# Kernel optimization log

Hardware: AMD Instinct MI355X
Metric: run time of the kernel (lower is better)

The kernel has to match this reference:

```python
import jax, jax.numpy as jnp
import numpy as np

NUM_TOKENS = 4096
LATENT_DIM = 128
BETA = 0.25
TEMP = 1.0  # temperature buffer (eval mode, no annealing)


def _l2_normalize(x, eps=1e-12):
    n = jnp.linalg.norm(x, axis=-1, keepdims=True)
    return x / jnp.maximum(n, eps)


def setup_inputs() -> dict:
    key = jax.random.key(0)
    k1, k2 = jax.random.split(key)
    latent = jax.random.normal(k1, (16, 1024, LATENT_DIM), dtype=jnp.float32)
    # codebook init: uniform(-1/num_tokens, 1/num_tokens) as in the module
    codebook_w = jax.random.uniform(
        k2, (NUM_TOKENS, LATENT_DIM), dtype=jnp.float32,
        minval=-1.0 / NUM_TOKENS, maxval=1.0 / NUM_TOKENS)
    return {"latent": latent, "codebook_w": codebook_w}


def reference(latent, codebook_w):
    B, S, D = latent.shape
    K = codebook_w.shape[0]
    flat = latent.reshape(-1, D)                      # [N, D]
    N = flat.shape[0]

    # cosine similarity between normalized inputs and codes
    cos = _l2_normalize(flat) @ _l2_normalize(codebook_w).T  # [N, K]

    # squared euclidean distances
    dist = (jnp.sum(flat * flat, axis=1, keepdims=True)
            - 2.0 * (flat @ codebook_w.T)
            + jnp.sum(codebook_w * codebook_w, axis=1))       # [N, K]

    soft = jax.nn.softmax(-dist / max(TEMP, 1e-5), axis=-1)   # [N, K]
    idx = jnp.argmax(soft, axis=-1)                            # [N]
    hard = jax.nn.one_hot(idx, K, dtype=flat.dtype)            # [N, K]
    # straight-through assignment
    assign = hard + soft - jax.lax.stop_gradient(soft)

    sel_cos = jnp.take_along_axis(cos, idx[:, None], axis=1).mean()

    # codebook self pairwise euclidean distances (K x K)
    sq = jnp.sum(codebook_w * codebook_w, axis=1)
    d2 = sq[:, None] + sq[None, :] - 2.0 * (codebook_w @ codebook_w.T)
    d = jnp.sqrt(jnp.maximum(d2, 0.0))
    # diagonal is exactly 0 after clamp, so off-diagonal mean = sum/(K*(K-1))
    avg_euclidean = d.sum() / (K * (K - 1))
    min_euclidean = jnp.min(jnp.where(jnp.eye(K, dtype=bool), jnp.inf, d))

    quantized = (assign @ codebook_w).reshape(B, S, D)
    commitment_loss = BETA * jnp.mean((jax.lax.stop_gradient(latent) - quantized) ** 2)
    codebook_loss = jnp.mean((latent - jax.lax.stop_gradient(quantized)) ** 2)
    quantized_st = latent + jax.lax.stop_gradient(quantized - latent)

    avg_probs = hard.mean(axis=0)
    perplexity = jnp.exp(-jnp.sum(avg_probs * jnp.log(avg_probs + 1e-10)))

    return (quantized_st, idx, commitment_loss, codebook_loss,
            perplexity, sel_cos, avg_euclidean, min_euclidean)
```

## Files before the change

kernel.cpp:

```cpp
#include <hip/hip_runtime.h>
#include <hip/hip_fp16.h>
#include <math.h>

#define NTOK 16384
#define KCB  4096
#define DIM  128
#define NG8  (KCB / 8)

typedef short bf16x8 __attribute__((ext_vector_type(8)));
typedef float f32x4  __attribute__((ext_vector_type(4)));

static __device__ inline unsigned short rne_bf16(float f) {
  unsigned u = __float_as_uint(f);
  return (unsigned short)((u + 0x7FFFu + ((u >> 16) & 1u)) >> 16);
}


__global__ __launch_bounds__(256) void k_convert(const float* __restrict__ cb,
                                                 unsigned short* __restrict__ cbh) {
  const int base = (blockIdx.x * 256 + threadIdx.x) * 8;
  float4 v0 = *(const float4*)(cb + base);
  float4 v1 = *(const float4*)(cb + base + 4);
  ushort4 o0, o1;
  o0.x = rne_bf16(v0.x); o0.y = rne_bf16(v0.y); o0.z = rne_bf16(v0.z); o0.w = rne_bf16(v0.w);
  o1.x = rne_bf16(v1.x); o1.y = rne_bf16(v1.y); o1.z = rne_bf16(v1.z); o1.w = rne_bf16(v1.w);
  *(ushort4*)(cbh + base) = o0;
  *(ushort4*)(cbh + base + 4) = o1;
}

__global__ __launch_bounds__(256) void k_rownorm(const float* __restrict__ lat,
                                                 const float* __restrict__ cb,
                                                 float* __restrict__ sumx2,
                                                 float* __restrict__ sumc2,
                                                 float* __restrict__ absum,
                                                 int* __restrict__ cnt) {
  if (blockIdx.x < 16) cnt[blockIdx.x * 256 + threadIdx.x] = 0;
  const int row  = blockIdx.x * 4 + (threadIdx.x >> 6);
  const int lane = threadIdx.x & 63;
  const float* src = (row < NTOK) ? (lat + (size_t)row * DIM)
                                  : (cb + (size_t)(row - NTOK) * DIM);
  float2 v = *(const float2*)(src + lane * 2);
  double s  = (double)v.x * (double)v.x + (double)v.y * (double)v.y;
  double sa = fabs((double)v.x) + fabs((double)v.y);
#pragma unroll
  for (int m = 32; m >= 1; m >>= 1) {
    s  += __shfl_xor(s, m, 64);
    sa += __shfl_xor(sa, m, 64);
  }
  if (lane == 0) {
    if (row < NTOK) { sumx2[row] = (float)s; absum[row] = (float)sa; }
    else            sumc2[row - NTOK] = (float)s;
  }
}

__global__ __launch_bounds__(256) void k_approx(const float* __restrict__ lat,
                                                const unsigned short* __restrict__ cbh,
                                                unsigned short* __restrict__ gmax8) {
  __shared__ __align__(16) unsigned char smem[16384];
  __shared__ __align__(16) unsigned short gbuf[256][72];
  const int t = threadIdx.x;
  const int w = t >> 6, l = t & 63;
  const int l15 = l & 15, lq = l >> 4;
  const int tokb = blockIdx.x * 256 + w * 64;
  const int ct0 = blockIdx.y * 4;

  bf16x8 bfr[4][4];
#pragma unroll
  for (int ctile = 0; ctile < 4; ++ctile) {
    const float* row = lat + (size_t)(tokb + ctile * 16 + l15) * DIM;
#pragma unroll
    for (int ks = 0; ks < 4; ++ks) {
      const int d0 = ks * 32 + lq * 4;
      float4 c0 = *(const float4*)(row + d0);
      float4 c1 = *(const float4*)(row + d0 + 16);
      union { ushort4 u4[2]; bf16x8 v; } cv;
      cv.u4[0].x = rne_bf16(c0.x); cv.u4[0].y = rne_bf16(c0.y);
      cv.u4[0].z = rne_bf16(c0.z); cv.u4[0].w = rne_bf16(c0.w);
      cv.u4[1].x = rne_bf16(c1.x); cv.u4[1].y = rne_bf16(c1.y);
      cv.u4[1].z = rne_bf16(c1.z); cv.u4[1].w = rne_bf16(c1.w);
      bfr[ctile][ks] = cv.v;
    }
  }

  for (int it = 0; it < 4; ++it) {
    const int ct = ct0 + it;
    __syncthreads();
    {
      const int r = t & 63, seg = t >> 6;
      const unsigned short* src = cbh + (size_t)(ct * 64 + r) * DIM + seg * 32;
      const int sw = (r & 7) << 4;
#pragma unroll
      for (int i = 0; i < 4; ++i) {
        uint4 v = *(const uint4*)(src + i * 8);
        *(uint4*)(smem + r * 256 + ((seg * 64 + i * 16) ^ sw)) = v;
      }
    }
    __syncthreads();

#pragma unroll
    for (int rt = 0; rt < 4; ++rt) {
      const int row = rt * 16 + l15;
      const int sw = (row & 7) << 4;
      bf16x8 afr[4];
#pragma unroll
      for (int ks = 0; ks < 4; ++ks) {
        const int off = ks * 64 + lq * 8;
        union { uint2 u2[2]; bf16x8 v; } cv;
        cv.u2[0] = *(const uint2*)(smem + row * 256 + (off ^ sw));
        cv.u2[1] = *(const uint2*)(smem + row * 256 + (((off + 32)) ^ sw));
        afr[ks] = cv.v;
      }
      f32x4 acc[4];
#pragma unroll
      for (int c = 0; c < 4; ++c) acc[c] = (f32x4){0.0f, 0.0f, 0.0f, 0.0f};
#pragma unroll
      for (int ks = 0; ks < 4; ++ks)
#pragma unroll
        for (int c = 0; c < 4; ++c)
          acc[c] = __builtin_amdgcn_mfma_f32_16x16x32_bf16(afr[ks], bfr[c][ks], acc[c], 0, 0, 0);
#pragma unroll
      for (int c = 0; c < 4; ++c) {
        const float gm = fmaxf(fmaxf(acc[c][0], acc[c][1]), fmaxf(acc[c][2], acc[c][3]));
        const int tokl = w * 64 + c * 16 + l15;
        gbuf[tokl][it * 16 + rt * 4 + lq] = __half_as_ushort(__float2half(gm));
      }
    }
  }

  __syncthreads();
  for (int c = t; c < 1024; c += 256) {
    const int token = c >> 2, seg = c & 3;
    const unsigned short* src = &gbuf[token][seg * 16];
    unsigned short in[16];
    *(uint4*)(in)     = *(const uint4*)(src);
    *(uint4*)(in + 8) = *(const uint4*)(src + 8);
    unsigned short o[8];
#pragma unroll
    for (int j = 0; j < 8; ++j) {
      const float f0 = __half2float(__ushort_as_half(in[2 * j]));
      const float f1 = __half2float(__ushort_as_half(in[2 * j + 1]));
      o[j] = __half_as_ushort(__float2half(fmaxf(f0, f1)));
    }
    *(uint4*)(gmax8 + (size_t)(blockIdx.x * 256 + token) * NG8 +
              blockIdx.y * 32 + seg * 8) = *(uint4*)o;
  }
}

__global__ __launch_bounds__(256) void k_resolve(const float* __restrict__ lat,
                                                 const float* __restrict__ cb,
                                                 const float* __restrict__ sumx2,
                                                 const float* __restrict__ sumc2,
                                                 const float* __restrict__ absum,
                                                 const unsigned short* __restrict__ gmax8,
                                                 float* __restrict__ qout,
                                                 float* __restrict__ idx_out,
                                                 float* __restrict__ msum,
                                                 float* __restrict__ csum,
                                                 int* __restrict__ cnt) {
  __shared__ __align__(16) float xs[4][DIM];
  __shared__ unsigned short q[4][NG8];
  __shared__ int qn[4];
  const int w = threadIdx.x >> 6, l = threadIdx.x & 63;
  const int tok = blockIdx.x * 4 + w;

  if (l == 0) qn[w] = 0;
  const float2 xv = *(const float2*)(lat + (size_t)tok * DIM + l * 2);
  const uint4 hv = *(const uint4*)(gmax8 + (size_t)tok * NG8 + l * 8);
  const float sx = sumx2[tok];
  const float ab = absum[tok];
  *(float2*)(&xs[w][l * 2]) = xv;

  float hf[8];
  hf[0] = __half2float(__ushort_as_half((unsigned short)(hv.x & 0xFFFFu)));
  hf[1] = __half2float(__ushort_as_half((unsigned short)(hv.x >> 16)));
  hf[2] = __half2float(__ushort_as_half((unsigned short)(hv.y & 0xFFFFu)));
  hf[3] = __half2float(__ushort_as_half((unsigned short)(hv.y >> 16)));
  hf[4] = __half2float(__ushort_as_half((unsigned short)(hv.z & 0xFFFFu)));
  hf[5] = __half2float(__ushort_as_half((unsigned short)(hv.z >> 16)));
  hf[6] = __half2float(__ushort_as_half((unsigned short)(hv.w & 0xFFFFu)));
  hf[7] = __half2float(__ushort_as_half((unsigned short)(hv.w >> 16)));
  float m = hf[0];
#pragma unroll
  for (int i = 1; i < 8; ++i) m = fmaxf(m, hf[i]);
#pragma unroll
  for (int s = 32; s >= 1; s >>= 1) m = fmaxf(m, __shfl_xor(m, s, 64));
  const float thr = m - (ab * 3.8224e-6f + 6.0e-5f);

  __syncthreads();
#pragma unroll
  for (int i = 0; i < 8; ++i) {
    if (hf[i] >= thr) {
      const int p = atomicAdd(&qn[w], 1);
      q[w][p] = (unsigned short)(l * 8 + i);
    }
  }
  __syncthreads();

  const int n = qn[w];
  const int slot = l >> 3, cidx = l & 7;
  unsigned long long bestp = ~0ull;
  const float4* xr4 = (const float4*)xs[w];

  for (int base = 0; base < n; base += 8) {
    unsigned long long pack = ~0ull;
    const int qi = base + slot;
    if (qi < n) {
      const int g = (int)q[w][qi];
      const int code = g * 8 + cidx;
      const float4* crow = (const float4*)(cb + (size_t)code * DIM);
      float acc = 0.0f;
#pragma unroll 8
      for (int ch = 0; ch < 32; ++ch) {
        const float4 c = crow[ch];
        const float4 x = xr4[ch];
        acc = fmaf(x.x, c.x, acc); acc = fmaf(x.y, c.y, acc);
        acc = fmaf(x.z, c.z, acc); acc = fmaf(x.w, c.w, acc);
      }
      const float dist = (sx - 2.0f * acc) + sumc2[code];
      pack = ((unsigned long long)__float_as_uint(dist) << 32) | (unsigned)code;
    }
#pragma unroll
    for (int s = 32; s >= 1; s >>= 1) {
      const unsigned long long o = __shfl_xor(pack, s, 64);
      pack = (o < pack) ? o : pack;
    }
    bestp = (pack < bestp) ? pack : bestp;
  }

  const int code = (int)(bestp & 0xFFFFFFFFull);
  const float2 c2 = *(const float2*)(cb + (size_t)code * DIM + l * 2);
  const float o0 = xv.x + (c2.x - xv.x);
  const float o1 = xv.y + (c2.y - xv.y);
  *(float2*)(qout + (size_t)tok * DIM + l * 2) = make_float2(o0, o1);
  const float e0 = xv.x - c2.x, e1 = xv.y - c2.y;
  float msel = e0 * e0 + e1 * e1;
  float dt = xv.x * c2.x + xv.y * c2.y;
#pragma unroll
  for (int s = 32; s >= 1; s >>= 1) {
    msel += __shfl_xor(msel, s, 64);
    dt += __shfl_xor(dt, s, 64);
  }
  if (l == 0) {
    const float nx = fmaxf(sqrtf(sx), 1e-12f);
    const float nc = fmaxf(sqrtf(sumc2[code]), 1e-12f);
    msum[tok] = msel;
    csum[tok] = dt / (nx * nc);
    idx_out[tok] = (float)code;
    atomicAdd(&cnt[code], 1);
  }
}

__global__ __launch_bounds__(256) void k_pair_mfma(const unsigned short* __restrict__ cbh,
                                                   const float* __restrict__ sumc2,
                                                   float* __restrict__ pairsum,
                                                   float* __restrict__ pairmin) {
  __shared__ __align__(16) unsigned char smem[16384];
  __shared__ float qs[64];
  const int t = threadIdx.x;
  const int w = t >> 6, l = t & 63;
  const int l15 = l & 15, lq = l >> 4;
  const int jb = blockIdx.x * 256 + w * 64;
  const int kb = blockIdx.y * 64;

  {
    const int r = t & 63, seg = t >> 6;
    const unsigned short* src = cbh + (size_t)(kb + r) * DIM + seg * 32;
    const int sw = (r & 7) << 4;
#pragma unroll
    for (int i = 0; i < 4; ++i) {
      uint4 v = *(const uint4*)(src + i * 8);
      *(uint4*)(smem + r * 256 + ((seg * 64 + i * 16) ^ sw)) = v;
    }
    if (t < 64) qs[t] = sumc2[kb + t];
  }

  bf16x8 bfr[4][4];
  float qj[4];
#pragma unroll
  for (int ct = 0; ct < 4; ++ct) {
    const unsigned short* rh = cbh + (size_t)(jb + ct * 16 + l15) * DIM;
#pragma unroll
    for (int ks = 0; ks < 4; ++ks) {
      const int d0 = ks * 32 + lq * 4;
      union { ushort4 u4[2]; bf16x8 v; } cvv;
      cvv.u4[0] = *(const ushort4*)(rh + d0);
      cvv.u4[1] = *(const ushort4*)(rh + d0 + 16);
      bfr[ct][ks] = cvv.v;
    }
    qj[ct] = sumc2[jb + ct * 16 + l15];
  }
  __syncthreads();

  float lsum = 0.0f, lmin = INFINITY;

#pragma unroll
  for (int rt = 0; rt < 4; ++rt) {
    const int row = rt * 16 + l15;
    const int sw = (row & 7) << 4;
    bf16x8 afr[4];
#pragma unroll
    for (int ks = 0; ks < 4; ++ks) {
      const int off = ks * 64 + lq * 8;
      union { uint2 u2[2]; bf16x8 v; } cv;
      cv.u2[0] = *(const uint2*)(smem + row * 256 + (off ^ sw));
      cv.u2[1] = *(const uint2*)(smem + row * 256 + (((off + 32)) ^ sw));
      afr[ks] = cv.v;
    }
    f32x4 acc[4];
#pragma unroll
    for (int c = 0; c < 4; ++c) acc[c] = (f32x4){0.0f, 0.0f, 0.0f, 0.0f};
#pragma unroll
    for (int ks = 0; ks < 4; ++ks)
#pragma unroll
      for (int c = 0; c < 4; ++c)
        acc[c] = __builtin_amdgcn_mfma_f32_16x16x32_bf16(afr[ks], bfr[c][ks], acc[c], 0, 0, 0);

#pragma unroll
    for (int c = 0; c < 4; ++c) {
      const int jg = jb + c * 16 + l15;
#pragma unroll
      for (int reg = 0; reg < 4; ++reg) {
        const int krl = rt * 16 + lq * 4 + reg;
        const int kg = kb + krl;
        const float d2 = (qj[c] + qs[krl]) - 2.0f * acc[c][reg];
        const float dd = sqrtf(fmaxf(d2, 0.0f));
        lsum += dd;
        if (jg != kg) lmin = fminf(lmin, dd);
      }
    }
  }

#pragma unroll
  for (int s = 32; s >= 1; s >>= 1) {
    lsum += __shfl_xor(lsum, s, 64);
    lmin = fminf(lmin, __shfl_xor(lmin, s, 64));
  }
  if (l == 0) {
    const int slot = (blockIdx.y * 16 + blockIdx.x) * 4 + w;
    pairsum[slot] = lsum;
    pairmin[slot] = lmin;
  }
}

__global__ __launch_bounds__(256) void k_final(const int* __restrict__ cnt,
                                               const float* __restrict__ msum,
                                               const float* __restrict__ csum,
                                               const float* __restrict__ pairsum,
                                               const float* __restrict__ pairmin,
                                               float* __restrict__ outs) {
  __shared__ float sh[256], sh2[256], sh3[256], sh4[256];
  const int t = threadIdx.x;
  float ent = 0.0f;
  for (int k = t; k < KCB; k += 256) {
    const float p = (float)cnt[k] * (1.0f / (float)NTOK);
    ent += p * logf(p + 1e-10f);
  }
  float ms = 0.0f, cs = 0.0f;
  for (int i = t; i < NTOK; i += 256) { ms += msum[i]; cs += csum[i]; }
  float ps = 0.0f, pm = INFINITY;
  for (int i = t; i < 4096; i += 256) { ps += pairsum[i]; pm = fminf(pm, pairmin[i]); }

  sh[t] = ent; sh2[t] = ms; sh3[t] = cs; sh4[t] = ps;
  __syncthreads();
  for (int s = 128; s >= 1; s >>= 1) {
    if (t < s) { sh[t] += sh[t + s]; sh2[t] += sh2[t + s];
                 sh3[t] += sh3[t + s]; sh4[t] += sh4[t + s]; }
    __syncthreads();
  }
  const float ent_tot = sh[0];
  const float ms_tot  = sh2[0];
  const float cs_tot  = sh3[0];
  const float ps_tot  = sh4[0];
  __syncthreads();
  sh[t] = pm;
  __syncthreads();
  for (int s = 128; s >= 1; s >>= 1) {
    if (t < s) sh[t] = fminf(sh[t], sh[t + s]);
    __syncthreads();
  }
  if (t == 0) {
    const float mse = ms_tot * (1.0f / (float)(NTOK * DIM));
    outs[0] = 0.25f * mse;
    outs[1] = mse;
    outs[2] = expf(-ent_tot);
    outs[3] = cs_tot * (1.0f / (float)NTOK);
    outs[4] = ps_tot / ((float)KCB * (float)(KCB - 1));
    outs[5] = sh[0];
  }
}

extern "C" void kernel_launch(void* const* d_in, const int* in_sizes, int n_in,
                              void* d_out, int out_size, void* d_ws, size_t ws_size,
                              hipStream_t stream) {
  const float* lat = (const float*)d_in[0];
  const float* cb  = (const float*)d_in[1];

  float* out     = (float*)d_out;
  float* qout    = out;
  float* idx_out = out + (size_t)NTOK * DIM;
  float* outs    = idx_out + NTOK;

  float* W        = (float*)d_ws;
  float* sumx2    = W;
  float* sumc2    = sumx2 + NTOK;
  float* absum    = sumc2 + KCB;
  int*   cnt      = (int*)(absum + NTOK);
  float* msum     = (float*)(cnt + KCB);
  float* csum     = msum + NTOK;
  float* pairsum  = csum + NTOK;
  float* pairmin  = pairsum + 4096;
  unsigned short* cbh   = (unsigned short*)(pairmin + 4096);
  unsigned short* gmax8 = cbh + (size_t)KCB * DIM;

  hipLaunchKernelGGL(k_convert, dim3(KCB * DIM / (256 * 8)), dim3(256), 0, stream,
                     cb, cbh);
  hipLaunchKernelGGL(k_rownorm, dim3((NTOK + KCB) / 4), dim3(256), 0, stream,
                     lat, cb, sumx2, sumc2, absum, cnt);
  hipLaunchKernelGGL(k_approx, dim3(NTOK / 256, 16), dim3(256), 0, stream,
                     lat, cbh, gmax8);
  hipLaunchKernelGGL(k_resolve, dim3(NTOK / 4), dim3(256), 0, stream,
                     lat, cb, sumx2, sumc2, absum, gmax8,
                     qout, idx_out, msum, csum, cnt);
  hipLaunchKernelGGL(k_pair_mfma, dim3(KCB / 256, KCB / 64), dim3(256), 0, stream,
                     cbh, sumc2, pairsum, pairmin);
  hipLaunchKernelGGL(k_final, dim3(1), dim3(256), 0, stream, cnt,
                     msum, csum, pairsum, pairmin, outs);
}
```

Baseline: 140.4 us.

## Shuffle-reduce group maxima, ballot-compact candidates, widen final reduction block

In the approximate scoring kernel, adjacent group maxima are now combined with a cross-lane shuffle before writing to shared memory. This halves the staging buffer and turns the epilogue into a plain copy. The resolve kernel replaces per-candidate shared-memory atomics and two block barriers with wave ballot and popcount prefix compaction. The single-block final reduction now uses 1024 threads instead of 256, giving fewer serial loads per thread but more reduction steps.

```diff
diff --git a/kernel.cpp b/kernel.cpp
--- a/kernel.cpp
+++ b/kernel.cpp
@@ -57,7 +57,7 @@
                                                 const unsigned short* __restrict__ cbh,
                                                 unsigned short* __restrict__ gmax8) {
   __shared__ __align__(16) unsigned char smem[16384];
-  __shared__ __align__(16) unsigned short gbuf[256][72];
+  __shared__ __align__(16) unsigned short gbuf[256][36];
   const int t = threadIdx.x;
   const int w = t >> 6, l = t & 63;
   const int l15 = l & 15, lq = l >> 4;
@@ -120,9 +120,13 @@
           acc[c] = __builtin_amdgcn_mfma_f32_16x16x32_bf16(afr[ks], bfr[c][ks], acc[c], 0, 0, 0);
 #pragma unroll
       for (int c = 0; c < 4; ++c) {
-        const float gm = fmaxf(fmaxf(acc[c][0], acc[c][1]), fmaxf(acc[c][2], acc[c][3]));
-        const int tokl = w * 64 + c * 16 + l15;
-        gbuf[tokl][it * 16 + rt * 4 + lq] = __half_as_ushort(__float2half(gm));
+        float gm = fmaxf(fmaxf(acc[c][0], acc[c][1]), fmaxf(acc[c][2], acc[c][3]));
+        gm = fmaxf(gm, __shfl_xor(gm, 16, 64));
+        if ((lq & 1) == 0) {
+          const int tokl = w * 64 + c * 16 + l15;
+          gbuf[tokl][it * 8 + rt * 2 + (lq >> 1)] =
+              __half_as_ushort(__float2half(gm));
+        }
       }
     }
   }
@@ -130,19 +134,11 @@
   __syncthreads();
   for (int c = t; c < 1024; c += 256) {
     const int token = c >> 2, seg = c & 3;
-    const unsigned short* src = &gbuf[token][seg * 16];
-    unsigned short in[16];
-    *(uint4*)(in)     = *(const uint4*)(src);
-    *(uint4*)(in + 8) = *(const uint4*)(src + 8);
-    unsigned short o[8];
-#pragma unroll
-    for (int j = 0; j < 8; ++j) {
-      const float f0 = __half2float(__ushort_as_half(in[2 * j]));
-      const float f1 = __half2float(__ushort_as_half(in[2 * j + 1]));
-      o[j] = __half_as_ushort(__float2half(fmaxf(f0, f1)));
-    }
+    uint2 a = *(const uint2*)(&gbuf[token][seg * 8]);
+    uint2 b = *(const uint2*)(&gbuf[token][seg * 8 + 4]);
+    uint4 o = make_uint4(a.x, a.y, b.x, b.y);
     *(uint4*)(gmax8 + (size_t)(blockIdx.x * 256 + token) * NG8 +
-              blockIdx.y * 32 + seg * 8) = *(uint4*)o;
+              blockIdx.y * 32 + seg * 8) = o;
   }
 }
 
@@ -159,11 +155,9 @@
                                                  int* __restrict__ cnt) {
   __shared__ __align__(16) float xs[4][DIM];
   __shared__ unsigned short q[4][NG8];
-  __shared__ int qn[4];
   const int w = threadIdx.x >> 6, l = threadIdx.x & 63;
   const int tok = blockIdx.x * 4 + w;
 
-  if (l == 0) qn[w] = 0;
   const float2 xv = *(const float2*)(lat + (size_t)tok * DIM + l * 2);
   const uint4 hv = *(const uint4*)(gmax8 + (size_t)tok * NG8 + l * 8);
   const float sx = sumx2[tok];
@@ -186,17 +180,16 @@
   for (int s = 32; s >= 1; s >>= 1) m = fmaxf(m, __shfl_xor(m, s, 64));
   const float thr = m - (ab * 3.8224e-6f + 6.0e-5f);
 
-  __syncthreads();
+  const unsigned long long ltm = (1ull << l) - 1ull;
+  int n = 0;
 #pragma unroll
   for (int i = 0; i < 8; ++i) {
-    if (hf[i] >= thr) {
-      const int p = atomicAdd(&qn[w], 1);
-      q[w][p] = (unsigned short)(l * 8 + i);
-    }
-  }
-  __syncthreads();
-
-  const int n = qn[w];
+    const bool f = (hf[i] >= thr);
+    const unsigned long long b = __ballot(f);
+    if (f) q[w][n + __popcll(b & ltm)] = (unsigned short)(l * 8 + i);
+    n += __popcll(b);
+  }
+
   const int slot = l >> 3, cidx = l & 7;
   unsigned long long bestp = ~0ull;
   const float4* xr4 = (const float4*)xs[w];
@@ -342,27 +335,27 @@
   }
 }
 
-__global__ __launch_bounds__(256) void k_final(const int* __restrict__ cnt,
-                                               const float* __restrict__ msum,
-                                               const float* __restrict__ csum,
-                                               const float* __restrict__ pairsum,
-                                               const float* __restrict__ pairmin,
-                                               float* __restrict__ outs) {
-  __shared__ float sh[256], sh2[256], sh3[256], sh4[256];
+__global__ __launch_bounds__(1024) void k_final(const int* __restrict__ cnt,
+                                                const float* __restrict__ msum,
+                                                const float* __restrict__ csum,
+                                                const float* __restrict__ pairsum,
+                                                const float* __restrict__ pairmin,
+                                                float* __restrict__ outs) {
+  __shared__ float sh[1024], sh2[1024], sh3[1024], sh4[1024];
   const int t = threadIdx.x;
   float ent = 0.0f;
-  for (int k = t; k < KCB; k += 256) {
+  for (int k = t; k < KCB; k += 1024) {
     const float p = (float)cnt[k] * (1.0f / (float)NTOK);
     ent += p * logf(p + 1e-10f);
   }
   float ms = 0.0f, cs = 0.0f;
-  for (int i = t; i < NTOK; i += 256) { ms += msum[i]; cs += csum[i]; }
+  for (int i = t; i < NTOK; i += 1024) { ms += msum[i]; cs += csum[i]; }
   float ps = 0.0f, pm = INFINITY;
-  for (int i = t; i < 4096; i += 256) { ps += pairsum[i]; pm = fminf(pm, pairmin[i]); }
+  for (int i = t; i < 4096; i += 1024) { ps += pairsum[i]; pm = fminf(pm, pairmin[i]); }
 
   sh[t] = ent; sh2[t] = ms; sh3[t] = cs; sh4[t] = ps;
   __syncthreads();
-  for (int s = 128; s >= 1; s >>= 1) {
+  for (int s = 512; s >= 1; s >>= 1) {
     if (t < s) { sh[t] += sh[t + s]; sh2[t] += sh2[t + s];
                  sh3[t] += sh3[t + s]; sh4[t] += sh4[t + s]; }
     __syncthreads();
@@ -374,7 +367,7 @@
   __syncthreads();
   sh[t] = pm;
   __syncthreads();
-  for (int s = 128; s >= 1; s >>= 1) {
+  for (int s = 512; s >= 1; s >>= 1) {
     if (t < s) sh[t] = fminf(sh[t], sh[t + s]);
     __syncthreads();
   }
@@ -423,6 +416,6 @@
                      qout, idx_out, msum, csum, cnt);
   hipLaunchKernelGGL(k_pair_mfma, dim3(KCB / 256, KCB / 64), dim3(256), 0, stream,
                      cbh, sumc2, pairsum, pairmin);
-  hipLaunchKernelGGL(k_final, dim3(1), dim3(256), 0, stream, cnt,
+  hipLaunchKernelGGL(k_final, dim3(1), dim3(1024), 0, stream, cnt,
                      msum, csum, pairsum, pairmin, outs);
 }
```

Result: faster. 128.5 us (-8.5%).
